# Kernel optimization log

Measured on AMD Instinct MI355X. Metric: run time of the kernel, lower is better.

## Reference

```python
import jax, jax.numpy as jnp
import numpy as np

EPS = 1e-6

def setup_inputs() -> dict:
    key = jax.random.key(0)
    k1, k2, k3 = jax.random.split(key, 3)
    B, T, D = 64, 2048, 768
    feature = jax.random.normal(k1, (B, T, D), dtype=jnp.float32)
    # base mask logits uniform in [0,1) (all non-negative)
    att_mask = jax.random.uniform(k2, (B, T, 1), dtype=jnp.float32)
    # emulate variable-length utterances: mark a random cutoff frame with a
    # negative logit for most samples (first negative index defines length-1)
    lengths = jax.random.randint(k3, (B,), T // 2, T)  # cutoff positions
    # leave a few samples with no negative entry (full-length path)
    lengths = jnp.where(jnp.arange(B) % 8 == 0, T + 1, lengths)
    t_idx = jnp.arange(T)[None, :]
    neg_marker = (t_idx == (lengths[:, None] - 1)).astype(jnp.float32)
    att_mask = att_mask - 2.0 * neg_marker[:, :, None]
    return {"feature": feature, "att_mask": att_mask}


def reference(feature, att_mask):
    # feature: [B, T, D]; att_mask: [B, T, 1]
    B, T, D = feature.shape
    neg = att_mask[:, :, 0] < 0                      # [B, T]
    has_neg = jnp.any(neg, axis=1)                   # [B]
    first_neg = jnp.argmax(neg, axis=1)              # [B] (0 if none)
    # original: length = first_negative_index + 1, else T
    length = jnp.where(has_neg, first_neg + 1, T)    # [B] int
    valid = (jnp.arange(T)[None, :] < length[:, None]).astype(feature.dtype)  # [B,T]
    inv_len = 1.0 / length.astype(feature.dtype)     # [B]
    # masked mean and mean-of-squares in one pass over feature
    mean_vec = jnp.einsum('btd,bt->bd', feature, valid) * inv_len[:, None]
    meansq = jnp.einsum('btd,bt->bd', feature * feature, valid) * inv_len[:, None]
    var_vec = jnp.sqrt(meansq - mean_vec * mean_vec + EPS)
    return jnp.concatenate([mean_vec, var_vec], axis=-1)  # [B, 2D]
```

## Files before the change

kernel.cpp:

```cpp
#include <hip/hip_runtime.h>
#include <math.h>

#define EPSV 1e-6f

__global__ void partial_kernel(const float* __restrict__ feat,
                               const float* __restrict__ mask,
                               int* __restrict__ lens,
                               float4* __restrict__ psum,
                               float4* __restrict__ psq,
                               int nchunk, int T, int D4) {
    const int c = blockIdx.x;
    const int b = blockIdx.y;

    const float* m = mask + (size_t)b * T;
    int local = T;
    for (int t = threadIdx.x; t < T; t += blockDim.x) {
        if (m[t] < 0.0f) local = min(local, t);
    }
    __shared__ int s[256];
    s[threadIdx.x] = local;
    if (threadIdx.x < 256 - 192) s[192 + threadIdx.x] = T;
    __syncthreads();
    #pragma unroll
    for (int off = 128; off > 0; off >>= 1) {
        if ((int)threadIdx.x < off)
            s[threadIdx.x] = min(s[threadIdx.x], s[threadIdx.x + off]);
        __syncthreads();
    }
    const int first = s[0];
    const int len = (first < T) ? (first + 1) : T;

    if (c == 0 && threadIdx.x == 0) lens[b] = len;

    const int t0 = (int)(((long long)c * len) / nchunk);
    const int t1 = (int)(((long long)(c + 1) * len) / nchunk);

    const float4* f = (const float4*)(feat + (size_t)b * T * (size_t)(D4 * 4));
    const int d4 = threadIdx.x;

    float4 sm = make_float4(0.f, 0.f, 0.f, 0.f);
    float4 sq = make_float4(0.f, 0.f, 0.f, 0.f);

    #pragma unroll 8
    for (int t = t0; t < t1; ++t) {
        float4 v = f[(size_t)t * D4 + d4];
        sm.x += v.x; sm.y += v.y; sm.z += v.z; sm.w += v.w;
        sq.x = fmaf(v.x, v.x, sq.x);
        sq.y = fmaf(v.y, v.y, sq.y);
        sq.z = fmaf(v.z, v.z, sq.z);
        sq.w = fmaf(v.w, v.w, sq.w);
    }

    const size_t idx = ((size_t)b * nchunk + c) * D4 + d4;
    psum[idx] = sm;
    psq[idx]  = sq;
}

__global__ void final_kernel(const float4* __restrict__ psum,
                             const float4* __restrict__ psq,
                             const int* __restrict__ lens,
                             float* __restrict__ out,
                             int nchunk, int D4) {
    const int b  = blockIdx.x;
    const int d4 = threadIdx.x;

    float4 s = make_float4(0.f, 0.f, 0.f, 0.f);
    float4 q = make_float4(0.f, 0.f, 0.f, 0.f);
    for (int c = 0; c < nchunk; ++c) {
        size_t idx = ((size_t)b * nchunk + c) * D4 + d4;
        float4 v = psum[idx];
        float4 w = psq[idx];
        s.x += v.x; s.y += v.y; s.z += v.z; s.w += v.w;
        q.x += w.x; q.y += w.y; q.z += w.z; q.w += w.w;
    }

    const float inv = 1.0f / (float)lens[b];
    float4 mean, var;
    mean.x = s.x * inv; mean.y = s.y * inv; mean.z = s.z * inv; mean.w = s.w * inv;
    var.x = sqrtf(fmaf(-mean.x, mean.x, q.x * inv) + EPSV);
    var.y = sqrtf(fmaf(-mean.y, mean.y, q.y * inv) + EPSV);
    var.z = sqrtf(fmaf(-mean.z, mean.z, q.z * inv) + EPSV);
    var.w = sqrtf(fmaf(-mean.w, mean.w, q.w * inv) + EPSV);

    const int D = D4 * 4;
    float4* orow = (float4*)(out + (size_t)b * 2 * D);
    orow[d4]      = mean;
    orow[D4 + d4] = var;
}

extern "C" void kernel_launch(void* const* d_in, const int* in_sizes, int n_in,
                              void* d_out, int out_size, void* d_ws, size_t ws_size,
                              hipStream_t stream) {
    const float* feature  = (const float*)d_in[0];
    const float* att_mask = (const float*)d_in[1];
    float* out = (float*)d_out;

    const int D  = (int)((long long)in_sizes[0] / in_sizes[1]);
    const int B  = out_size / (2 * D);
    const int T  = in_sizes[1] / B;
    const int D4 = D / 4;

    int* lens = (int*)d_ws;
    const size_t per_chunk_bytes = (size_t)B * D4 * sizeof(float4) * 2;
    int nchunk = 16;
    if (ws_size >= 4096 + per_chunk_bytes) {
        int fit = (int)((ws_size - 4096) / per_chunk_bytes);
        if (fit < nchunk) nchunk = fit;
    } else {
        nchunk = 1;
    }
    if (nchunk < 1) nchunk = 1;

    float4* psum = (float4*)((char*)d_ws + 4096);
    float4* psq  = psum + (size_t)B * nchunk * D4;

    dim3 grid(nchunk, B);
    partial_kernel<<<grid, D4, 0, stream>>>(feature, att_mask, lens, psum, psq,
                                            nchunk, T, D4);
    final_kernel<<<B, D4, 0, stream>>>(psum, psq, lens, out, nchunk, D4);
}
```

Before: 67.94 us.

## Split length scan into own kernel and use atomic work-queue persistent blocks

Moves the per-batch first-negative scan into a separate len_kernel so each partial block no longer rescans the mask row. The partial kernel becomes a persistent grid of 1024 blocks that pull (batch, chunk) work units from an atomic counter, with chunks per batch raised from 16 to 32. This is meant to cut redundant mask reads and balance load across the uneven sequence lengths. It costs an extra kernel launch and some atomic and barrier overhead per unit.

```diff
diff --git a/kernel.cpp b/kernel.cpp
--- a/kernel.cpp
+++ b/kernel.cpp
@@ -3,15 +3,10 @@
 
 #define EPSV 1e-6f
 
-__global__ void partial_kernel(const float* __restrict__ feat,
-                               const float* __restrict__ mask,
-                               int* __restrict__ lens,
-                               float4* __restrict__ psum,
-                               float4* __restrict__ psq,
-                               int nchunk, int T, int D4) {
-    const int c = blockIdx.x;
-    const int b = blockIdx.y;
-
+__global__ void len_kernel(const float* __restrict__ mask,
+                           int* __restrict__ lens, int* __restrict__ ctr,
+                           int T, int seed) {
+    const int b = blockIdx.x;
     const float* m = mask + (size_t)b * T;
     int local = T;
     for (int t = threadIdx.x; t < T; t += blockDim.x) {
@@ -19,7 +14,6 @@
     }
     __shared__ int s[256];
     s[threadIdx.x] = local;
-    if (threadIdx.x < 256 - 192) s[192 + threadIdx.x] = T;
     __syncthreads();
     #pragma unroll
     for (int off = 128; off > 0; off >>= 1) {
@@ -27,47 +21,69 @@
             s[threadIdx.x] = min(s[threadIdx.x], s[threadIdx.x + off]);
         __syncthreads();
     }
-    const int first = s[0];
-    const int len = (first < T) ? (first + 1) : T;
+    if (threadIdx.x == 0) {
+        int first = s[0];
+        lens[b] = (first < T) ? (first + 1) : T;
+        if (b == 0) ctr[0] = seed;
+    }
+}
 
-    if (c == 0 && threadIdx.x == 0) lens[b] = len;
+__global__ void partial_kernel(const float* __restrict__ feat,
+                               const int* __restrict__ lens,
+                               int* __restrict__ ctr,
+                               float4* __restrict__ psum,
+                               float4* __restrict__ psq,
+                               int CPB, int NU, int T, int D4) {
+    __shared__ int s_next;
+    const int d4 = threadIdx.x;
+    int unit = blockIdx.x;
 
-    const int t0 = (int)(((long long)c * len) / nchunk);
-    const int t1 = (int)(((long long)(c + 1) * len) / nchunk);
+    while (unit < NU) {
+        __syncthreads();
+        if (threadIdx.x == 0) s_next = atomicAdd(ctr, 1);
 
-    const float4* f = (const float4*)(feat + (size_t)b * T * (size_t)(D4 * 4));
-    const int d4 = threadIdx.x;
+        const int b = unit / CPB;
+        const int c = unit - b * CPB;
+        const int len = lens[b];
+        const int t0 = (int)(((long long)c * len) / CPB);
+        const int t1 = (int)(((long long)(c + 1) * len) / CPB);
 
-    float4 sm = make_float4(0.f, 0.f, 0.f, 0.f);
-    float4 sq = make_float4(0.f, 0.f, 0.f, 0.f);
+        const float4* f = (const float4*)feat + (size_t)b * T * D4;
 
-    #pragma unroll 8
-    for (int t = t0; t < t1; ++t) {
-        float4 v = f[(size_t)t * D4 + d4];
-        sm.x += v.x; sm.y += v.y; sm.z += v.z; sm.w += v.w;
-        sq.x = fmaf(v.x, v.x, sq.x);
-        sq.y = fmaf(v.y, v.y, sq.y);
-        sq.z = fmaf(v.z, v.z, sq.z);
-        sq.w = fmaf(v.w, v.w, sq.w);
+        float4 sm = make_float4(0.f, 0.f, 0.f, 0.f);
+        float4 sq = make_float4(0.f, 0.f, 0.f, 0.f);
+
+        #pragma unroll 8
+        for (int t = t0; t < t1; ++t) {
+            float4 v = f[(size_t)t * D4 + d4];
+            sm.x += v.x; sm.y += v.y; sm.z += v.z; sm.w += v.w;
+            sq.x = fmaf(v.x, v.x, sq.x);
+            sq.y = fmaf(v.y, v.y, sq.y);
+            sq.z = fmaf(v.z, v.z, sq.z);
+            sq.w = fmaf(v.w, v.w, sq.w);
+        }
+
+        const size_t idx = (size_t)unit * D4 + d4;
+        psum[idx] = sm;
+        psq[idx]  = sq;
+
+        __syncthreads();
+        unit = s_next;
     }
-
-    const size_t idx = ((size_t)b * nchunk + c) * D4 + d4;
-    psum[idx] = sm;
-    psq[idx]  = sq;
 }
 
 __global__ void final_kernel(const float4* __restrict__ psum,
                              const float4* __restrict__ psq,
                              const int* __restrict__ lens,
                              float* __restrict__ out,
-                             int nchunk, int D4) {
+                             int CPB, int D4) {
     const int b  = blockIdx.x;
     const int d4 = threadIdx.x;
 
     float4 s = make_float4(0.f, 0.f, 0.f, 0.f);
     float4 q = make_float4(0.f, 0.f, 0.f, 0.f);
-    for (int c = 0; c < nchunk; ++c) {
-        size_t idx = ((size_t)b * nchunk + c) * D4 + d4;
+    for (int c = 0; c < CPB; ++c) {
+        size_t idx = ((size_t)b * CPB + c) * D4 + d4;
         float4 v = psum[idx];
         float4 w = psq[idx];
         s.x += v.x; s.y += v.y; s.z += v.z; s.w += v.w;
@@ -100,22 +116,27 @@
     const int T  = in_sizes[1] / B;
     const int D4 = D / 4;
 
-    int* lens = (int*)d_ws;
+    int* ctr  = (int*)d_ws;
+    int* lens = (int*)((char*)d_ws + 256);
+
     const size_t per_chunk_bytes = (size_t)B * D4 * sizeof(float4) * 2;
-    int nchunk = 16;
+    int CPB = 32;
     if (ws_size >= 4096 + per_chunk_bytes) {
         int fit = (int)((ws_size - 4096) / per_chunk_bytes);
-        if (fit < nchunk) nchunk = fit;
+        if (fit < CPB) CPB = fit;
     } else {
-        nchunk = 1;
+        CPB = 1;
     }
-    if (nchunk < 1) nchunk = 1;
+    if (CPB < 1) CPB = 1;
+    const int NU = B * CPB;
 
     float4* psum = (float4*)((char*)d_ws + 4096);
-    float4* psq  = psum + (size_t)B * nchunk * D4;
+    float4* psq  = psum + (size_t)NU * D4;
 
-    dim3 grid(nchunk, B);
-    partial_kernel<<<grid, D4, 0, stream>>>(feature, att_mask, lens, psum, psq,
-                                            nchunk, T, D4);
-    final_kernel<<<B, D4, 0, stream>>>(psum, psq, lens, out, nchunk, D4);
+    const int NB = 1024;
+
+    len_kernel<<<B, 256, 0, stream>>>(att_mask, lens, ctr, T, NB);
+    partial_kernel<<<NB, D4, 0, stream>>>(feature, lens, ctr, psum, psq,
+                                          CPB, NU, T, D4);
+    final_kernel<<<B, D4, 0, stream>>>(psum, psq, lens, out, CPB, D4);
 }
```

Measured after the change: 85.06 us. +25.2%, slower.

## Split length scan into own kernel and raise chunk count for more parallelism

Applied to the files above, without the earlier changes.

Moves the per-sample first-negative mask scan out of every partial block into a separate vectorized len_kernel, so each of the nchunk blocks no longer rescans the whole mask row. Raises the number of time chunks from 16 to up to 64 (subject to workspace size), giving more blocks to spread the memory-bound feature reduction across CUs. In exchange it adds a third kernel launch and a larger partials buffer that the final kernel must read back, and it adds launch bounds and unrolling to the final reduction.

```diff
diff --git a/kernel.cpp b/kernel.cpp
--- a/kernel.cpp
+++ b/kernel.cpp
@@ -3,23 +3,27 @@
 
 #define EPSV 1e-6f
 
-__global__ void partial_kernel(const float* __restrict__ feat,
-                               const float* __restrict__ mask,
-                               int* __restrict__ lens,
-                               float4* __restrict__ psum,
-                               float4* __restrict__ psq,
-                               int nchunk, int T, int D4) {
-    const int c = blockIdx.x;
-    const int b = blockIdx.y;
-
+__global__ void len_kernel(const float* __restrict__ mask,
+                           int* __restrict__ lens, int T) {
+    const int b = blockIdx.x;
     const float* m = mask + (size_t)b * T;
     int local = T;
-    for (int t = threadIdx.x; t < T; t += blockDim.x) {
-        if (m[t] < 0.0f) local = min(local, t);
+    if ((T & 3) == 0) {
+        const float4* m4 = (const float4*)m;
+        const int T4 = T >> 2;
+        for (int i = threadIdx.x; i < T4; i += blockDim.x) {
+            float4 v = m4[i];
+            if (v.x < 0.f) local = min(local, 4 * i);
+            if (v.y < 0.f) local = min(local, 4 * i + 1);
+            if (v.z < 0.f) local = min(local, 4 * i + 2);
+            if (v.w < 0.f) local = min(local, 4 * i + 3);
+        }
+    } else {
+        for (int t = threadIdx.x; t < T; t += blockDim.x)
+            if (m[t] < 0.f) local = min(local, t);
     }
     __shared__ int s[256];
     s[threadIdx.x] = local;
-    if (threadIdx.x < 256 - 192) s[192 + threadIdx.x] = T;
     __syncthreads();
     #pragma unroll
     for (int off = 128; off > 0; off >>= 1) {
@@ -27,15 +31,25 @@
             s[threadIdx.x] = min(s[threadIdx.x], s[threadIdx.x + off]);
         __syncthreads();
     }
-    const int first = s[0];
-    const int len = (first < T) ? (first + 1) : T;
+    if (threadIdx.x == 0) {
+        int first = s[0];
+        lens[b] = (first < T) ? (first + 1) : T;
+    }
+}
 
-    if (c == 0 && threadIdx.x == 0) lens[b] = len;
-
+__global__ __launch_bounds__(192) void partial_kernel(
+        const float* __restrict__ feat,
+        const int* __restrict__ lens,
+        float4* __restrict__ psum,
+        float4* __restrict__ psq,
+        int nchunk, int T, int D4) {
+    const int c = blockIdx.x;
+    const int b = blockIdx.y;
+    const int len = lens[b];
     const int t0 = (int)(((long long)c * len) / nchunk);
     const int t1 = (int)(((long long)(c + 1) * len) / nchunk);
 
-    const float4* f = (const float4*)(feat + (size_t)b * T * (size_t)(D4 * 4));
+    const float4* f = (const float4*)feat + (size_t)b * T * D4;
     const int d4 = threadIdx.x;
 
     float4 sm = make_float4(0.f, 0.f, 0.f, 0.f);
@@ -51,25 +65,29 @@
         sq.w = fmaf(v.w, v.w, sq.w);
     }
 
-    const size_t idx = ((size_t)b * nchunk + c) * D4 + d4;
-    psum[idx] = sm;
-    psq[idx]  = sq;
+    const size_t slot = ((size_t)b * nchunk + c) * D4 + d4;
+    psum[slot] = sm;
+    psq[slot]  = sq;
 }
 
-__global__ void final_kernel(const float4* __restrict__ psum,
-                             const float4* __restrict__ psq,
-                             const int* __restrict__ lens,
-                             float* __restrict__ out,
-                             int nchunk, int D4) {
+__global__ __launch_bounds__(192) void final_kernel(
+        const float4* __restrict__ psum,
+        const float4* __restrict__ psq,
+        const int* __restrict__ lens,
+        float* __restrict__ out,
+        int nchunk, int D4) {
     const int b  = blockIdx.x;
     const int d4 = threadIdx.x;
 
+    const float4* ps = psum + (size_t)b * nchunk * D4 + d4;
+    const float4* pq = psq  + (size_t)b * nchunk * D4 + d4;
+
     float4 s = make_float4(0.f, 0.f, 0.f, 0.f);
     float4 q = make_float4(0.f, 0.f, 0.f, 0.f);
+    #pragma unroll 4
     for (int c = 0; c < nchunk; ++c) {
-        size_t idx = ((size_t)b * nchunk + c) * D4 + d4;
-        float4 v = psum[idx];
-        float4 w = psq[idx];
+        float4 v = ps[(size_t)c * D4];
+        float4 w = pq[(size_t)c * D4];
         s.x += v.x; s.y += v.y; s.z += v.z; s.w += v.w;
         q.x += w.x; q.y += w.y; q.z += w.z; q.w += w.w;
     }
@@ -100,22 +118,22 @@
     const int T  = in_sizes[1] / B;
     const int D4 = D / 4;
 
-    int* lens = (int*)d_ws;
-    const size_t per_chunk_bytes = (size_t)B * D4 * sizeof(float4) * 2;
-    int nchunk = 16;
-    if (ws_size >= 4096 + per_chunk_bytes) {
-        int fit = (int)((ws_size - 4096) / per_chunk_bytes);
-        if (fit < nchunk) nchunk = fit;
-    } else {
-        nchunk = 1;
+    int nchunk = 64;
+    size_t need;
+    for (;;) {
+        const size_t NS = (size_t)B * nchunk;
+        need = 4096 + NS * D4 * sizeof(float4) * 2;
+        if (need <= ws_size || nchunk <= 1) break;
+        nchunk >>= 1;
     }
-    if (nchunk < 1) nchunk = 1;
 
+    int*    lens = (int*)d_ws;
     float4* psum = (float4*)((char*)d_ws + 4096);
     float4* psq  = psum + (size_t)B * nchunk * D4;
 
+    len_kernel<<<B, 256, 0, stream>>>(att_mask, lens, T);
     dim3 grid(nchunk, B);
-    partial_kernel<<<grid, D4, 0, stream>>>(feature, att_mask, lens, psum, psq,
+    partial_kernel<<<grid, D4, 0, stream>>>(feature, lens, psum, psq,
                                             nchunk, T, D4);
     final_kernel<<<B, D4, 0, stream>>>(psum, psq, lens, out, nchunk, D4);
 }
```

New measurement: 77.78 us. +14.5%, slower.
